# Kernel optimization log

Measured on AMD Instinct MI355X. Metric: run time of the kernel, lower is better.

The kernel has to match this reference:

```python
import jax, jax.numpy as jnp
import numpy as np

B, T, D, R = 16, 4096, 512, 256

# Buffers (match torch: linspace(0,T-1,R).long() truncates toward zero)
_LANDMARKS = np.linspace(0.0, T - 1, R).astype(np.int64)
_POS = np.arange(T)[:, None]                                   # [T,1]
_MASK = (_LANDMARKS[None, :] < _POS)                           # [T,R] bool: landmark j < position i
_TDIST = np.clip((_POS.astype(np.float32) - _LANDMARKS[None, :].astype(np.float32)) / T, 0.0, None).astype(np.float32)  # [T,R]


def setup_inputs() -> dict:
    key = jax.random.key(0)
    k1, k2, k3 = jax.random.split(key, 3)
    return {
        "z": jax.random.normal(k1, (B, T, D), dtype=jnp.float32),
        "gegenbauer_weights": jax.random.normal(k2, (3,), dtype=jnp.float32),
        "temporal_alpha": jax.random.normal(k3, (1,), dtype=jnp.float32),
    }


def reference(z, gegenbauer_weights, temporal_alpha):
    dtype = z.dtype
    mask = jnp.asarray(_MASK)                       # [T,R]
    tdist = jnp.asarray(_TDIST, dtype=dtype)        # [T,R]
    lm = jnp.asarray(_LANDMARKS)                    # [R]

    # F.normalize(z, dim=-1) with eps=1e-12
    norm = jnp.linalg.norm(z, axis=-1, keepdims=True)
    Q = z / jnp.maximum(norm, 1e-12)                # [B,T,D]
    K = Q[:, lm, :]                                 # [B,R,D]
    C = jnp.einsum('btd,brd->btr', Q, K)            # [B,T,R] cosine similarity

    # Gegenbauer mixture
    alpha = jax.nn.softmax(gegenbauer_weights)
    C2 = C * C
    P1 = (1.0 + C) * 0.5
    P2 = (3.0 * C2 - 1.0) * 0.5
    P3 = (5.0 * C2 * C - 3.0 * C) * 0.5
    Phi = alpha[0] * P1 + alpha[1] * P2 + alpha[2] * P3

    # Causal mask
    Phi = Phi * mask.astype(dtype)[None, :, :]

    # Temporal decay
    a_td = jax.nn.softplus(temporal_alpha[0])
    Phi = Phi * jnp.exp(-a_td * tdist)[None, :, :]

    # Row-sum normalization
    row_sum = jnp.maximum(Phi.sum(axis=-1, keepdims=True), 1e-6)
    Phi = Phi / row_sum

    # Append constant-ones feature -> [B,T,R+1]
    ones = jnp.ones((Phi.shape[0], Phi.shape[1], 1), dtype=dtype)
    return jnp.concatenate([Phi, ones], axis=-1)
```

## Files before the change

### kernel.cpp

```cpp
#include <hip/hip_runtime.h>
#include <hip/hip_bf16.h>
#include <math.h>

#define B_DIM 16
#define T_DIM 4096
#define D_DIM 512
#define R_DIM 256

#define TM 64
#define BK 64
#define LDP 72
#define NKS (D_DIM/32)

typedef __bf16 bf16x8 __attribute__((ext_vector_type(8)));
typedef float floatx4 __attribute__((ext_vector_type(4)));

__device__ __forceinline__ int landmark_of(int r) {
    if (r >= 255) return 4095;
    const double step = 4095.0 / 255.0;
    return (int)((double)r * step);
}

__device__ __forceinline__ void split_bf16(float x, __bf16& h, __bf16& l) {
    h = (__bf16)x;
    l = (__bf16)(x - (float)h);
}

__global__ void nystrom_prep_kernel(const float* __restrict__ z,
                                    __bf16* __restrict__ Khi, __bf16* __restrict__ Klo) {
    int blk = blockIdx.x;
    int b = blk >> 8;
    int r = blk & 255;
    int lane = threadIdx.x;
    int lm = landmark_of(r);
    const float* src = z + ((size_t)b * T_DIM + lm) * D_DIM + lane * 8;
    float4 v0 = ((const float4*)src)[0];
    float4 v1 = ((const float4*)src)[1];
    float ss = v0.x*v0.x + v0.y*v0.y + v0.z*v0.z + v0.w*v0.w
             + v1.x*v1.x + v1.y*v1.y + v1.z*v1.z + v1.w*v1.w;
    #pragma unroll
    for (int off = 1; off < 64; off <<= 1) ss += __shfl_xor(ss, off, 64);
    float inv = 1.0f / fmaxf(sqrtf(ss), 1e-12f);
    float q[8] = {v0.x*inv, v0.y*inv, v0.z*inv, v0.w*inv,
                  v1.x*inv, v1.y*inv, v1.z*inv, v1.w*inv};
    bf16x8 oh, ol;
    #pragma unroll
    for (int j = 0; j < 8; j++) { __bf16 h, l; split_bf16(q[j], h, l); oh[j] = h; ol[j] = l; }
    size_t dst = ((((size_t)b * NKS + (lane >> 2)) * 16 + (r >> 4)) * 64
                  + (size_t)(lane & 3) * 16 + (r & 15)) * 8;
    *(bf16x8*)(Khi + dst) = oh;
    *(bf16x8*)(Klo + dst) = ol;
}

__global__ __launch_bounds__(256, 3)
void nystrom_main_kernel(const float* __restrict__ z,
                         const __bf16* __restrict__ Khi, const __bf16* __restrict__ Klo,
                         const float* __restrict__ gw, const float* __restrict__ ta,
                         float* __restrict__ out) {
    __shared__ __attribute__((aligned(16))) char smem[36864];
    __shared__ int   lmtab[R_DIM];
    __shared__ float elmtab[R_DIM];

    float* red    = (float*)(smem);
    float* rnormp = (float*)(smem + 1024);
    float* rinvp  = (float*)(smem + 1280);
    float* rspart = (float*)(smem + 1536);

    const int tid  = threadIdx.x;
    const int b    = blockIdx.y;
    const int t0   = blockIdx.x * TM;
    const int lane = tid & 63;
    const int wv   = tid >> 6;
    const int quad = lane >> 4;
    const int ln   = lane & 15;

    float g0 = gw[0], g1 = gw[1], g2 = gw[2];
    float gm = fmaxf(g0, fmaxf(g1, g2));
    float e0 = expf(g0 - gm), e1 = expf(g1 - gm), e2 = expf(g2 - gm);
    float esum = e0 + e1 + e2;
    float al0 = e0 / esum, al1 = e1 / esum, al2 = e2 / esum;
    float ax = ta[0];
    float a_td = (ax > 20.f) ? ax : log1pf(expf(ax));

    {
        int lm = landmark_of(tid);
        lmtab[tid] = lm;
        elmtab[tid] = expf(a_td * (float)lm * (1.0f / 4096.0f));
    }

    const int srowA = tid >> 2;
    const int scolA = (tid & 3) * 16;
    const float* zrow = z + ((size_t)b * T_DIM + (t0 + srowA)) * D_DIM + scolA;

    const size_t kfoff = (size_t)b * (NKS * 16 * 64 * 8)
                       + (size_t)wv * 2048 + (size_t)lane * 8;
    const __bf16* khb = Khi + kfoff;
    const __bf16* klb = Klo + kfoff;

    floatx4 acc[4][4];
    #pragma unroll
    for (int i = 0; i < 4; i++)
        #pragma unroll
        for (int j = 0; j < 4; j++) acc[i][j] = (floatx4){0.f, 0.f, 0.f, 0.f};
    float ssq = 0.0f;

    float4 a0, a1, a2, a3;

    {
        const float4* ap = (const float4*)(zrow);
        a0 = ap[0]; a1 = ap[1]; a2 = ap[2]; a3 = ap[3];
        float av[16] = {a0.x,a0.y,a0.z,a0.w, a1.x,a1.y,a1.z,a1.w,
                        a2.x,a2.y,a2.z,a2.w, a3.x,a3.y,a3.z,a3.w};
        #pragma unroll
        for (int j = 0; j < 16; j++) ssq += av[j] * av[j];
        __bf16* wsh = (__bf16*)(smem);
        __bf16* wsl = (__bf16*)(smem + 9216);
        #pragma unroll
        for (int g = 0; g < 2; g++) {
            bf16x8 ph, pl;
            #pragma unroll
            for (int j = 0; j < 8; j++) {
                __bf16 h, l; split_bf16(av[g*8+j], h, l); ph[j] = h; pl[j] = l;
            }
            *(bf16x8*)&wsh[srowA * LDP + scolA + g*8] = ph;
            *(bf16x8*)&wsl[srowA * LDP + scolA + g*8] = pl;
        }
    }
    __syncthreads();

    #pragma unroll 1
    for (int kt = 0; kt < D_DIM; kt += BK) {
        const int cur = (kt >> 6) & 1;
        const bool has_next = (kt + BK < D_DIM);

        if (has_next) {
            const float4* ap = (const float4*)(zrow + kt + BK);
            a0 = ap[0]; a1 = ap[1]; a2 = ap[2]; a3 = ap[3];
        }

        const __bf16* Ash = (const __bf16*)(smem + cur * 18432);
        const __bf16* Asl = (const __bf16*)(smem + cur * 18432 + 9216);
        const int ksb = kt >> 5;
        #pragma unroll
        for (int s = 0; s < 2; s++) {
            const __bf16* khp = khb + (size_t)(ksb + s) * 8192;
            const __bf16* klp = klb + (size_t)(ksb + s) * 8192;
            bf16x8 bh[4], bl[4];
            #pragma unroll
            for (int ni = 0; ni < 4; ni++) {
                bh[ni] = *(const bf16x8*)(khp + ni * 512);
                bl[ni] = *(const bf16x8*)(klp + ni * 512);
            }
            const int koff = s * 32 + quad * 8;
            #pragma unroll
            for (int mi = 0; mi < 4; mi++) {
                bf16x8 afh = *(const bf16x8*)&Ash[(mi * 16 + ln) * LDP + koff];
                bf16x8 afl = *(const bf16x8*)&Asl[(mi * 16 + ln) * LDP + koff];
                #pragma unroll
                for (int ni = 0; ni < 4; ni++) {
                    acc[mi][ni] = __builtin_amdgcn_mfma_f32_16x16x32_bf16(
                        afh, bh[ni], acc[mi][ni], 0, 0, 0);
                    acc[mi][ni] = __builtin_amdgcn_mfma_f32_16x16x32_bf16(
                        afh, bl[ni], acc[mi][ni], 0, 0, 0);
                    acc[mi][ni] = __builtin_amdgcn_mfma_f32_16x16x32_bf16(
                        afl, bh[ni], acc[mi][ni], 0, 0, 0);
                }
            }
        }

        if (has_next) {
            float av[16] = {a0.x,a0.y,a0.z,a0.w, a1.x,a1.y,a1.z,a1.w,
                            a2.x,a2.y,a2.z,a2.w, a3.x,a3.y,a3.z,a3.w};
            #pragma unroll
            for (int j = 0; j < 16; j++) ssq += av[j] * av[j];
            __bf16* wsh = (__bf16*)(smem + (cur ^ 1) * 18432);
            __bf16* wsl = (__bf16*)(smem + (cur ^ 1) * 18432 + 9216);
            #pragma unroll
            for (int g = 0; g < 2; g++) {
                bf16x8 ph, pl;
                #pragma unroll
                for (int j = 0; j < 8; j++) {
                    __bf16 h, l; split_bf16(av[g*8+j], h, l); ph[j] = h; pl[j] = l;
                }
                *(bf16x8*)&wsh[srowA * LDP + scolA + g*8] = ph;
                *(bf16x8*)&wsl[srowA * LDP + scolA + g*8] = pl;
            }
        }
        __syncthreads();
    }

    red[tid] = ssq;
    __syncthreads();
    if (tid < TM) {
        float s = red[tid * 4] + red[tid * 4 + 1] + red[tid * 4 + 2] + red[tid * 4 + 3];
        rnormp[tid] = 1.0f / fmaxf(sqrtf(s), 1e-12f);
    }
    __syncthreads();

    int   lm_r[4];
    float elm_r[4];
    #pragma unroll
    for (int ni = 0; ni < 4; ni++) {
        int r = wv * 64 + ni * 16 + ln;
        lm_r[ni]  = lmtab[r];
        elm_r[ni] = elmtab[r];
    }

    #pragma unroll
    for (int mi = 0; mi < 4; mi++) {
        #pragma unroll
        for (int reg = 0; reg < 4; reg++) {
            int row = mi * 16 + quad * 4 + reg;
            int t = t0 + row;
            float rn = rnormp[row];
            float e_t = expf(-a_td * (float)t * (1.0f / 4096.0f));
            float s = 0.f;
            #pragma unroll
            for (int ni = 0; ni < 4; ni++) {
                float phi = 0.f;
                if (lm_r[ni] < t) {
                    float c  = acc[mi][ni][reg] * rn;
                    float c2 = c * c;
                    float P1 = 0.5f * (1.f + c);
                    float P2 = 0.5f * (3.f * c2 - 1.f);
                    float P3 = 0.5f * (5.f * c2 * c - 3.f * c);
                    float p  = al0 * P1 + al1 * P2 + al2 * P3;
                    phi = p * e_t * elm_r[ni];
                }
                acc[mi][ni][reg] = phi;
                s += phi;
            }
            #pragma unroll
            for (int off = 1; off < 16; off <<= 1) s += __shfl_xor(s, off, 64);
            if (ln == 0) rspart[wv * TM + row] = s;
        }
    }
    __syncthreads();
    if (tid < TM) {
        float rs = rspart[0 * TM + tid] + rspart[1 * TM + tid]
                 + rspart[2 * TM + tid] + rspart[3 * TM + tid];
        rinvp[tid] = 1.0f / fmaxf(rs, 1e-6f);
    }
    __syncthreads();

    float* ob = out + ((size_t)b * T_DIM + t0) * 257;
    #pragma unroll
    for (int mi = 0; mi < 4; mi++) {
        #pragma unroll
        for (int reg = 0; reg < 4; reg++) {
            int row = mi * 16 + quad * 4 + reg;
            float inv = rinvp[row];
            #pragma unroll
            for (int ni = 0; ni < 4; ni++) {
                int r = wv * 64 + ni * 16 + ln;
                ob[(size_t)row * 257 + r] = acc[mi][ni][reg] * inv;
            }
        }
    }
    if (tid < TM) ob[(size_t)tid * 257 + 256] = 1.0f;
}

extern "C" void kernel_launch(void* const* d_in, const int* in_sizes, int n_in,
                              void* d_out, int out_size, void* d_ws, size_t ws_size,
                              hipStream_t stream) {
    const float* z  = (const float*)d_in[0];
    const float* gw = (const float*)d_in[1];
    const float* ta = (const float*)d_in[2];
    float* out = (float*)d_out;
    __bf16* Khi = (__bf16*)d_ws;
    __bf16* Klo = (__bf16*)((char*)d_ws + (size_t)B_DIM * R_DIM * D_DIM * 2);

    nystrom_prep_kernel<<<dim3(B_DIM * R_DIM), 64, 0, stream>>>(z, Khi, Klo);
    nystrom_main_kernel<<<dim3(T_DIM / TM, B_DIM), 256, 0, stream>>>(z, Khi, Klo, gw, ta, out);
}
```

Measured before the change: 259.6 us.

## Skip causally masked landmark tiles and interleave column mapping across waves

```diff
diff --git a/kernel.cpp b/kernel.cpp
--- a/kernel.cpp
+++ b/kernel.cpp
@@ -52,6 +52,33 @@
     *(bf16x8*)(Klo + dst) = ol;
 }
 
+template<int NACT>
+__device__ __forceinline__ void mfma_phase(const __bf16* __restrict__ Ash,
+                                           const __bf16* __restrict__ Asl,
+                                           const __bf16* __restrict__ khp,
+                                           const __bf16* __restrict__ klp,
+                                           int koff, int ln, floatx4 (&acc)[4][4]) {
+    bf16x8 bh[NACT], bl[NACT];
+    #pragma unroll
+    for (int ni = 0; ni < NACT; ni++) {
+        bh[ni] = *(const bf16x8*)(khp + ni * 2048);
+        bl[ni] = *(const bf16x8*)(klp + ni * 2048);
+    }
+    __builtin_amdgcn_s_setprio(1);
+    #pragma unroll
+    for (int mi = 0; mi < 4; mi++) {
+        bf16x8 afh = *(const bf16x8*)&Ash[(mi * 16 + ln) * LDP + koff];
+        bf16x8 afl = *(const bf16x8*)&Asl[(mi * 16 + ln) * LDP + koff];
+        #pragma unroll
+        for (int ni = 0; ni < NACT; ni++) {
+            acc[mi][ni] = __builtin_amdgcn_mfma_f32_16x16x32_bf16(afh, bh[ni], acc[mi][ni], 0, 0, 0);
+            acc[mi][ni] = __builtin_amdgcn_mfma_f32_16x16x32_bf16(afh, bl[ni], acc[mi][ni], 0, 0, 0);
+            acc[mi][ni] = __builtin_amdgcn_mfma_f32_16x16x32_bf16(afl, bh[ni], acc[mi][ni], 0, 0, 0);
+        }
+    }
+    __builtin_amdgcn_s_setprio(0);
+}
+
 __global__ __launch_bounds__(256, 3)
 void nystrom_main_kernel(const float* __restrict__ z,
                          const __bf16* __restrict__ Khi, const __bf16* __restrict__ Klo,
@@ -88,12 +115,17 @@
         elmtab[tid] = expf(a_td * (float)lm * (1.0f / 4096.0f));
     }
 
+    int nact = 0;
+    #pragma unroll
+    for (int ni = 0; ni < 4; ni++)
+        if (landmark_of(ni * 64 + wv * 16) < t0 + TM - 1) nact = ni + 1;
+
     const int srowA = tid >> 2;
     const int scolA = (tid & 3) * 16;
     const float* zrow = z + ((size_t)b * T_DIM + (t0 + srowA)) * D_DIM + scolA;
 
     const size_t kfoff = (size_t)b * (NKS * 16 * 64 * 8)
-                       + (size_t)wv * 2048 + (size_t)lane * 8;
+                       + (size_t)wv * 512 + (size_t)lane * 8;
     const __bf16* khb = Khi + kfoff;
     const __bf16* klb = Klo + kfoff;
 
@@ -145,26 +177,13 @@
         for (int s = 0; s < 2; s++) {
             const __bf16* khp = khb + (size_t)(ksb + s) * 8192;
             const __bf16* klp = klb + (size_t)(ksb + s) * 8192;
-            bf16x8 bh[4], bl[4];
-            #pragma unroll
-            for (int ni = 0; ni < 4; ni++) {
-                bh[ni] = *(const bf16x8*)(khp + ni * 512);
-                bl[ni] = *(const bf16x8*)(klp + ni * 512);
-            }
             const int koff = s * 32 + quad * 8;
-            #pragma unroll
-            for (int mi = 0; mi < 4; mi++) {
-                bf16x8 afh = *(const bf16x8*)&Ash[(mi * 16 + ln) * LDP + koff];
-                bf16x8 afl = *(const bf16x8*)&Asl[(mi * 16 + ln) * LDP + koff];
-                #pragma unroll
-                for (int ni = 0; ni < 4; ni++) {
-                    acc[mi][ni] = __builtin_amdgcn_mfma_f32_16x16x32_bf16(
-                        afh, bh[ni], acc[mi][ni], 0, 0, 0);
-                    acc[mi][ni] = __builtin_amdgcn_mfma_f32_16x16x32_bf16(
-                        afh, bl[ni], acc[mi][ni], 0, 0, 0);
-                    acc[mi][ni] = __builtin_amdgcn_mfma_f32_16x16x32_bf16(
-                        afl, bh[ni], acc[mi][ni], 0, 0, 0);
-                }
+            switch (nact) {
+                case 4: mfma_phase<4>(Ash, Asl, khp, klp, koff, ln, acc); break;
+                case 3: mfma_phase<3>(Ash, Asl, khp, klp, koff, ln, acc); break;
+                case 2: mfma_phase<2>(Ash, Asl, khp, klp, koff, ln, acc); break;
+                case 1: mfma_phase<1>(Ash, Asl, khp, klp, koff, ln, acc); break;
+                default: break;
             }
         }
 
@@ -201,7 +220,7 @@
     float elm_r[4];
     #pragma unroll
     for (int ni = 0; ni < 4; ni++) {
-        int r = wv * 64 + ni * 16 + ln;
+        int r = ni * 64 + wv * 16 + ln;
         lm_r[ni]  = lmtab[r];
         elm_r[ni] = elmtab[r];
     }
@@ -213,7 +232,7 @@
             int row = mi * 16 + quad * 4 + reg;
             int t = t0 + row;
             float rn = rnormp[row];
-            float e_t = expf(-a_td * (float)t * (1.0f / 4096.0f));
+            float e_t = __expf(-a_td * (float)t * (1.0f / 4096.0f));
             float s = 0.f;
             #pragma unroll
             for (int ni = 0; ni < 4; ni++) {
@@ -252,7 +271,7 @@
             float inv = rinvp[row];
             #pragma unroll
             for (int ni = 0; ni < 4; ni++) {
-                int r = wv * 64 + ni * 16 + ln;
+                int r = ni * 64 + wv * 16 + ln;
                 ob[(size_t)row * 257 + r] = acc[mi][ni][reg] * inv;
             }
         }
```

Measured after the change: 262.2 us. Within noise of the previous version (+1.0%).
